# Kernel optimization log

Measured on AMD Instinct MI355X. Metric: run time of the kernel, lower is better.

The kernel has to match this reference:

```python
import jax, jax.numpy as jnp
import numpy as np

N, D, E, TOP_K = 2048, 512, 16, 2
HID = 4 * D
EPS = 1e-10


def setup_inputs() -> dict:
    key = jax.random.key(0)
    ks = jax.random.split(key, 8)
    s = 0.02
    return {
        "x": jax.random.normal(ks[0], (N, D), dtype=jnp.float32),
        "w_norm": jnp.ones((D,), dtype=jnp.float32),
        "Wr": jax.random.normal(ks[1], (D, E), dtype=jnp.float32) * s,
        "br": jnp.zeros((E,), dtype=jnp.float32),
        "W1": jax.random.normal(ks[2], (E, D, HID), dtype=jnp.float32) * s,
        "b1": jnp.zeros((E, HID), dtype=jnp.float32),
        "W2": jax.random.normal(ks[3], (E, HID, D), dtype=jnp.float32) * s,
        "b2": jnp.zeros((E, D), dtype=jnp.float32),
    }


def reference(x, w_norm, Wr, br, W1, b1, W2, b2):
    res = x
    # RMSNorm over feature dim (dim=1 in the torch code for 2D input)
    rms = jnp.sqrt(jnp.mean(x * x, axis=1, keepdims=True) + EPS)
    xn = w_norm * (x / rms)
    # Router: top-k over expert logits, softmax over the k selected logits
    logits = xn @ Wr + br                      # [N, E]
    top_p, top_i = jax.lax.top_k(logits, TOP_K)  # [N, k]
    top_p = jax.nn.softmax(top_p, axis=-1)
    # Dense per-token expert weights [N, E] (top-k indices are distinct)
    weight = jnp.zeros((x.shape[0], E), dtype=x.dtype)
    weight = weight.at[jnp.arange(x.shape[0])[:, None], top_i].add(top_p)
    # All-expert FFN (dense reference for the routed dispatch)
    h = jnp.einsum("nd,edh->enh", xn, W1) + b1[:, None, :]   # [E, N, 4D]
    y = jnp.einsum("enh,ehd->end", jax.nn.silu(h), W2) + b2[:, None, :]  # [E, N, D]
    out = jnp.einsum("end,ne->nd", y, weight)
    return out + res
```

## Files before the change

kernel.cpp:

```cpp
#include <hip/hip_runtime.h>

#define N_TOK 2048
#define DIM   512
#define NEXP  16
#define HID   2048
#define NSLOT (N_TOK*2)

typedef __attribute__((ext_vector_type(8))) short short8;
typedef __attribute__((ext_vector_type(4))) float floatx4;

__device__ __forceinline__ ushort f2bf(float f) {
    union { float f; unsigned u; } c; c.f = f;
    unsigned u = c.u;
    unsigned r = (u + 0x7fffu + ((u >> 16) & 1u)) >> 16;
    return (ushort)r;
}

__device__ __forceinline__ void gl_lds16(const void* g, void* l) {
    __builtin_amdgcn_global_load_lds(
        (const __attribute__((address_space(1))) unsigned int*)g,
        (__attribute__((address_space(3))) unsigned int*)l, 16, 0, 0);
}

__global__ __launch_bounds__(256)
void transpose_convert(const float* __restrict__ src, ushort* __restrict__ dst,
                       int K, int Nn)
{
    const int NT = Nn >> 6, KT = K >> 6;
    int bx = blockIdx.x;
    const int nt = bx % NT; bx /= NT;
    const int kt = bx % KT; bx /= KT;
    const int e  = bx;

    __shared__ float Ls[64 * 65];
    const int t = threadIdx.x;

    const float* sp = src + ((size_t)e * K + kt * 64) * Nn + nt * 64;
#pragma unroll
    for (int i = 0; i < 4; i++) {
        const int k  = (t >> 4) + i * 16;
        const int c4 = (t & 15) * 4;
        const float4 v = *(const float4*)(sp + (size_t)k * Nn + c4);
        Ls[k * 65 + c4 + 0] = v.x;
        Ls[k * 65 + c4 + 1] = v.y;
        Ls[k * 65 + c4 + 2] = v.z;
        Ls[k * 65 + c4 + 3] = v.w;
    }
    __syncthreads();

    ushort* dp = dst + ((size_t)e * Nn + nt * 64) * K + kt * 64;
#pragma unroll
    for (int i = 0; i < 2; i++) {
        const int n = (t >> 3) + i * 32;
        const int c = t & 7;
        unsigned w[4];
#pragma unroll
        for (int q = 0; q < 4; q++) {
            const unsigned lo = f2bf(Ls[(c * 8 + q * 2 + 0) * 65 + n]);
            const unsigned hi = f2bf(Ls[(c * 8 + q * 2 + 1) * 65 + n]);
            w[q] = lo | (hi << 16);
        }
        uint4 o = make_uint4(w[0], w[1], w[2], w[3]);
        *(uint4*)(dp + (size_t)n * K + c * 8) = o;
    }
}

__global__ __launch_bounds__(256)
void router_fused(const float* __restrict__ x, const float* __restrict__ w_norm,
                  const float* __restrict__ Wr, const float* __restrict__ br,
                  ushort* __restrict__ xn, int2* __restrict__ rec_e,
                  float2* __restrict__ rec_w)
{
    __shared__ float xs[16][516];
    __shared__ float wrT[16][516];

    const int tid  = threadIdx.x;
    const int wave = tid >> 6, lane = tid & 63;
    const int tblk = blockIdx.x * 16;

#pragma unroll
    for (int k = 0; k < 32; k++) {
        const int idx = tid + k * 256;
        wrT[idx & 15][idx >> 4] = Wr[idx];
    }

    const float4* wnp = (const float4*)w_norm;
    const float4 wa = wnp[lane], wb = wnp[lane + 64];
#pragma unroll
    for (int i = 0; i < 4; i++) {
        const int tl = wave * 4 + i, t = tblk + tl;
        const float4* xp = (const float4*)(x + (size_t)t * DIM);
        const float4 a = xp[lane], b = xp[lane + 64];
        float ss = a.x*a.x + a.y*a.y + a.z*a.z + a.w*a.w
                 + b.x*b.x + b.y*b.y + b.z*b.z + b.w*b.w;
#pragma unroll
        for (int m = 32; m >= 1; m >>= 1) ss += __shfl_xor(ss, m, 64);
        const float rinv = 1.f / sqrtf(ss * (1.f / (float)DIM) + 1e-10f);
        float4 na, nb;
        na.x = a.x * wa.x * rinv; na.y = a.y * wa.y * rinv;
        na.z = a.z * wa.z * rinv; na.w = a.w * wa.w * rinv;
        nb.x = b.x * wb.x * rinv; nb.y = b.y * wb.y * rinv;
        nb.z = b.z * wb.z * rinv; nb.w = b.w * wb.w * rinv;
        *(float4*)&xs[tl][lane * 4]       = na;
        *(float4*)&xs[tl][256 + lane * 4] = nb;
        ushort4 ua, ub;
        ua.x = f2bf(na.x); ua.y = f2bf(na.y); ua.z = f2bf(na.z); ua.w = f2bf(na.w);
        ub.x = f2bf(nb.x); ub.y = f2bf(nb.y); ub.z = f2bf(nb.z); ub.w = f2bf(nb.w);
        ushort4* xo = (ushort4*)(xn + (size_t)t * DIM);
        xo[lane] = ua; xo[lane + 64] = ub;
    }
    __syncthreads();

    const int tl = tid >> 4, e = tid & 15;
    const int t = tblk + tl;
    float acc = 0.f;
#pragma unroll 4
    for (int d = 0; d < DIM; d += 4) {
        const float4 xv = *(const float4*)&xs[tl][d];
        const float4 wv = *(const float4*)&wrT[e][d];
        acc += xv.x * wv.x + xv.y * wv.y + xv.z * wv.z + xv.w * wv.w;
    }
    const float v = acc + br[e];

    float m0 = v; int i0 = e; float m1 = -1e30f; int i1 = 16;
#pragma unroll
    for (int msk = 1; msk < 16; msk <<= 1) {
        const float om0 = __shfl_xor(m0, msk, 64); const int oi0 = __shfl_xor(i0, msk, 64);
        const float om1 = __shfl_xor(m1, msk, 64); const int oi1 = __shfl_xor(i1, msk, 64);
        const bool bf_ = (om0 > m0) || (om0 == m0 && oi0 < i0);
        const float t0m = bf_ ? om0 : m0; const int t0i = bf_ ? oi0 : i0;
        const float l0m = bf_ ? m0 : om0; const int l0i = bf_ ? i0 : oi0;
        const bool b2_ = (om1 > m1) || (om1 == m1 && oi1 < i1);
        const float t2m = b2_ ? om1 : m1; const int t2i = b2_ ? oi1 : i1;
        const bool lw = (l0m > t2m) || (l0m == t2m && l0i < t2i);
        m0 = t0m; i0 = t0i;
        m1 = lw ? l0m : t2m; i1 = lw ? l0i : t2i;
    }
    if (e == 0) {
        const float ex = expf(m1 - m0);
        const float w0 = 1.f / (1.f + ex);
        rec_e[t] = make_int2(i0, i1);
        rec_w[t] = make_float2(w0, ex * w0);
    }
}

__global__ __launch_bounds__(1024)
void plan_kernel(const int2* __restrict__ rec_e, int* __restrict__ cnt,
                 int* __restrict__ off, int* __restrict__ tok_of_slot,
                 int* __restrict__ rec_slot)
{
    __shared__ int soff[17];
    const int e = threadIdx.x >> 6;
    const int lane = threadIdx.x & 63;

    int total = 0;
    for (int c = 0; c < N_TOK / 64; c++) {
        const int2 er = rec_e[c * 64 + lane];
        const bool hit = (er.x == e) || (er.y == e);
        total += __popcll(__ballot(hit));
    }
    if (lane == 0) soff[e + 1] = total;
    __syncthreads();
    if (threadIdx.x == 0) {
        soff[0] = 0;
        for (int q = 1; q <= 16; q++) soff[q] += soff[q - 1];
    }
    __syncthreads();
    int base = soff[e];
    if (lane == 0) { cnt[e] = soff[e + 1] - base; off[e] = base; }

    for (int c = 0; c < N_TOK / 64; c++) {
        const int t = c * 64 + lane;
        const int2 er = rec_e[t];
        const bool hit = (er.x == e) || (er.y == e);
        const unsigned long long b = __ballot(hit);
        if (hit) {
            const int slot = base + __popcll(b & ((1ull << lane) - 1ull));
            tok_of_slot[slot] = t;
            const int which = (er.y == e) ? 1 : 0;
            rec_slot[t * 2 + which] = slot;
        }
        base += __popcll(b);
    }
}

template<int MODE>
__global__ __launch_bounds__(256)
void gemm_expert(const ushort* __restrict__ A, int a_stride,
                 const ushort* __restrict__ WT, int wt_k,
                 const float* __restrict__ bias,
                 const int* __restrict__ cnt, const int* __restrict__ off,
                 const int* __restrict__ tok_of_slot,
                 ushort* __restrict__ hout, float* __restrict__ yout)
{
    const int flat = blockIdx.x + (blockIdx.y << 5);
    const int x = flat & 7;
    const int g = flat >> 3;
    int e, mt, nb, z;
    if (MODE == 0) {
        e  = x + ((g >> 7) << 3);
        const int r = g & 127;
        nb = r & 31; mt = r >> 5; z = 0;
    } else {
        const int G = ((g >> 5) << 3) + x;
        e = G >> 2; z = G & 3;
        const int idx = g & 31;
        mt = idx >> 3; nb = idx & 7;
    }

    const int count = cnt[e];
    if (mt * 128 >= count) return;
    const int base = off[e];
    const int rows = min(128, count - mt * 128);
    const int n0   = nb * 64;
    const int Nn   = (MODE == 0) ? HID : DIM;
    const int kbeg = (MODE == 0) ? 0 : (z * 512);
    float* yp = (MODE == 0) ? nullptr : (yout + (size_t)z * NSLOT * DIM);

    __shared__ __align__(16) ushort As[2][128 * 64];
    __shared__ __align__(16) ushort Bs[2][64 * 64];
    __shared__ int toks[128];

    const int tid = threadIdx.x;
    if (tid < 128) {
        const int r = tid < rows ? tid : rows - 1;
        const int slot = base + mt * 128 + r;
        toks[tid] = (MODE == 0) ? tok_of_slot[slot] : slot;
    }
    __syncthreads();

    const int lane = tid & 63;
    const int wid  = tid >> 6;
    const int wm = wid >> 1, wn = wid & 1;
    const int fr = lane & 15, fg = lane >> 4;

    const int lrow = lane >> 3;
    const int sch  = (lane & 7) ^ lrow;

    const ushort* aptr[4];
#pragma unroll
    for (int j = 0; j < 4; j++) {
        const int s = wid * 4 + j;
        aptr[j] = A + (size_t)toks[s * 8 + lrow] * a_stride + sch * 8;
    }
    const ushort* wbase = WT + (size_t)e * Nn * wt_k + (size_t)n0 * wt_k;
    const ushort* bptr[2];
#pragma unroll
    for (int j = 0; j < 2; j++) {
        const int s = wid * 2 + j;
        bptr[j] = wbase + (size_t)(s * 8 + lrow) * wt_k + sch * 8;
    }

    floatx4 acc[4][2];
#pragma unroll
    for (int mi = 0; mi < 4; mi++)
#pragma unroll
        for (int ni = 0; ni < 2; ni++)
#pragma unroll
            for (int r = 0; r < 4; r++) acc[mi][ni][r] = 0.f;

#define STAGE(pb, k0)                                                        \
    do {                                                                     \
        _Pragma("unroll")                                                    \
        for (int j = 0; j < 4; j++)                                          \
            gl_lds16(aptr[j] + (k0), (void*)(&As[pb][(wid * 4 + j) * 512])); \
        _Pragma("unroll")                                                    \
        for (int j = 0; j < 2; j++)                                          \
            gl_lds16(bptr[j] + (k0), (void*)(&Bs[pb][(wid * 2 + j) * 512])); \
    } while (0)

    int cur = 0;
    STAGE(0, kbeg);

    for (int kt = 0; kt < 8; kt++) {
        if (kt < 7) {
            STAGE(cur ^ 1, kbeg + (kt + 1) * 64);
            asm volatile("s_waitcnt vmcnt(6)" ::: "memory");
        } else {
            asm volatile("s_waitcnt vmcnt(0)" ::: "memory");
        }
        __builtin_amdgcn_s_barrier();
        __builtin_amdgcn_sched_barrier(0);

#pragma unroll
        for (int kh = 0; kh < 2; kh++) {
            const int co = ((kh * 4 + fg) ^ (fr & 7)) * 8;
            short8 af[4], bfr[2];
#pragma unroll
            for (int mi = 0; mi < 4; mi++)
                af[mi] = *(const short8*)&As[cur][(wm * 64 + mi * 16 + fr) * 64 + co];
#pragma unroll
            for (int ni = 0; ni < 2; ni++)
                bfr[ni] = *(const short8*)&Bs[cur][(wn * 32 + ni * 16 + fr) * 64 + co];
#pragma unroll
            for (int mi = 0; mi < 4; mi++)
#pragma unroll
                for (int ni = 0; ni < 2; ni++)
                    acc[mi][ni] = __builtin_amdgcn_mfma_f32_16x16x32_bf16(af[mi], bfr[ni], acc[mi][ni], 0, 0, 0);
        }

        __builtin_amdgcn_sched_barrier(0);
        __builtin_amdgcn_s_barrier();
        cur ^= 1;
    }
#undef STAGE

#pragma unroll
    for (int ni = 0; ni < 2; ni++) {
        const int gn = n0 + wn * 32 + ni * 16 + fr;
        const float bv = (MODE == 0) ? bias[e * HID + gn] : 0.f;
#pragma unroll
        for (int mi = 0; mi < 4; mi++) {
#pragma unroll
            for (int r = 0; r < 4; r++) {
                const int lm = wm * 64 + mi * 16 + fg * 4 + r;
                if (lm < rows) {
                    const int slot = base + mt * 128 + lm;
                    float v = acc[mi][ni][r];
                    if (MODE == 0) {
                        v += bv;
                        v = v / (1.f + expf(-v));
                        hout[(size_t)slot * HID + gn] = f2bf(v);
                    } else {
                        yp[(size_t)slot * DIM + gn] = v;
                    }
                }
            }
        }
    }
}

__global__ __launch_bounds__(128)
void gather_kernel(const float* __restrict__ x, const float* __restrict__ ypart,
                   const float* __restrict__ b2,
                   const int2* __restrict__ rec_e, const float2* __restrict__ rec_w,
                   const int2* __restrict__ rec_slot, float* __restrict__ out)
{
    const int t = blockIdx.x;
    const int d4 = threadIdx.x * 4;
    const int2 ei = rec_e[t];
    const float2 w = rec_w[t];
    const int2 sl = rec_slot[t];
    const float4 xv  = *(const float4*)(x  + (size_t)t * DIM + d4);
    float4 s0 = make_float4(0.f, 0.f, 0.f, 0.f);
    float4 s1 = make_float4(0.f, 0.f, 0.f, 0.f);
#pragma unroll
    for (int kc = 0; kc < 4; kc++) {
        const float* yp = ypart + (size_t)kc * NSLOT * DIM;
        const float4 a = *(const float4*)(yp + (size_t)sl.x * DIM + d4);
        const float4 b = *(const float4*)(yp + (size_t)sl.y * DIM + d4);
        s0.x += a.x; s0.y += a.y; s0.z += a.z; s0.w += a.w;
        s1.x += b.x; s1.y += b.y; s1.z += b.z; s1.w += b.w;
    }
    const float4 b0  = *(const float4*)(b2 + (size_t)ei.x * DIM + d4);
    const float4 b1v = *(const float4*)(b2 + (size_t)ei.y * DIM + d4);
    float4 o;
    o.x = xv.x + w.x * (s0.x + b0.x) + w.y * (s1.x + b1v.x);
    o.y = xv.y + w.x * (s0.y + b0.y) + w.y * (s1.y + b1v.y);
    o.z = xv.z + w.x * (s0.z + b0.z) + w.y * (s1.z + b1v.z);
    o.w = xv.w + w.x * (s0.w + b0.w) + w.y * (s1.w + b1v.w);
    *(float4*)(out + (size_t)t * DIM + d4) = o;
}

extern "C" void kernel_launch(void* const* d_in, const int* in_sizes, int n_in,
                              void* d_out, int out_size, void* d_ws, size_t ws_size,
                              hipStream_t stream)
{
    const float* x  = (const float*)d_in[0];
    const float* wn = (const float*)d_in[1];
    const float* Wr = (const float*)d_in[2];
    const float* br = (const float*)d_in[3];
    const float* W1 = (const float*)d_in[4];
    const float* b1 = (const float*)d_in[5];
    const float* W2 = (const float*)d_in[6];
    const float* b2 = (const float*)d_in[7];
    float* out = (float*)d_out;

    char* ws = (char*)d_ws;
    ushort* W1T   = (ushort*)(ws);
    ushort* W2T   = (ushort*)(ws + (32u << 20));
    ushort* xn    = (ushort*)(ws + (64u << 20));
    ushort* h_buf = (ushort*)(ws + (66u << 20));
    float*  y_par = (float*) (ws + (82u << 20));
    char* p = ws + (114u << 20);
    int*    cnt         = (int*)p;    p += 256;
    int*    off         = (int*)p;    p += 256;
    int2*   rec_e       = (int2*)p;   p += N_TOK * 8;
    float2* rec_w       = (float2*)p; p += N_TOK * 8;
    int2*   rec_slot    = (int2*)p;   p += N_TOK * 8;
    int*    tok_of_slot = (int*)p;    p += NSLOT * 4;

    router_fused<<<N_TOK / 16, 256, 0, stream>>>(x, wn, Wr, br, xn, rec_e, rec_w);
    plan_kernel<<<1, 1024, 0, stream>>>(rec_e, cnt, off, tok_of_slot, (int*)rec_slot);

    transpose_convert<<<NEXP * 8 * 32, 256, 0, stream>>>(W1, W1T, DIM, HID);
    gemm_expert<0><<<dim3(32, 64), 256, 0, stream>>>(
        xn, DIM, W1T, DIM, b1, cnt, off, tok_of_slot, h_buf, nullptr);

    transpose_convert<<<NEXP * 32 * 8, 256, 0, stream>>>(W2, W2T, HID, DIM);
    gemm_expert<1><<<dim3(32, 64), 256, 0, stream>>>(
        h_buf, HID, W2T, HID, nullptr, cnt, off, nullptr, nullptr, y_par);

    gather_kernel<<<N_TOK, 128, 0, stream>>>(x, y_par, b2, rec_e, rec_w, rec_slot, out);
}
```

Baseline: 119.2 us.

## Halve GEMM K-tile to 32, store split-K partials in bf16, use fast exp

The expert GEMM k-tile drops from 64 to 32, so the loop runs twice as many iterations with half the LDS per stage. The LDS swizzle and the load mapping are reworked to match, and s_setprio is raised around the MFMA block. The split-K partial outputs of the second GEMM are now stored as bf16 instead of fp32, which halves the partial-sum write and read traffic in the gather kernel at some cost in precision. SiLU switches to __expf.

```diff
diff --git a/kernel.cpp b/kernel.cpp
--- a/kernel.cpp
+++ b/kernel.cpp
@@ -14,6 +14,10 @@
     unsigned u = c.u;
     unsigned r = (u + 0x7fffu + ((u >> 16) & 1u)) >> 16;
     return (ushort)r;
+}
+__device__ __forceinline__ float bf2f(ushort u) {
+    union { unsigned u; float f; } c; c.u = ((unsigned)u) << 16;
+    return c.f;
 }
 
 __device__ __forceinline__ void gl_lds16(const void* g, void* l) {
@@ -191,7 +195,7 @@
                  const float* __restrict__ bias,
                  const int* __restrict__ cnt, const int* __restrict__ off,
                  const int* __restrict__ tok_of_slot,
-                 ushort* __restrict__ hout, float* __restrict__ yout)
+                 ushort* __restrict__ hout, ushort* __restrict__ yout)
 {
     const int flat = blockIdx.x + (blockIdx.y << 5);
     const int x = flat & 7;
@@ -215,10 +219,10 @@
     const int n0   = nb * 64;
     const int Nn   = (MODE == 0) ? HID : DIM;
     const int kbeg = (MODE == 0) ? 0 : (z * 512);
-    float* yp = (MODE == 0) ? nullptr : (yout + (size_t)z * NSLOT * DIM);
-
-    __shared__ __align__(16) ushort As[2][128 * 64];
-    __shared__ __align__(16) ushort Bs[2][64 * 64];
+    ushort* yp = (MODE == 0) ? nullptr : (yout + (size_t)z * NSLOT * DIM);
+
+    __shared__ __align__(16) ushort As[2][128 * 32];
+    __shared__ __align__(16) ushort Bs[2][64 * 32];
     __shared__ int toks[128];
 
     const int tid = threadIdx.x;
@@ -234,22 +238,17 @@
     const int wm = wid >> 1, wn = wid & 1;
     const int fr = lane & 15, fg = lane >> 4;
 
-    const int lrow = lane >> 3;
-    const int sch  = (lane & 7) ^ lrow;
-
-    const ushort* aptr[4];
-#pragma unroll
-    for (int j = 0; j < 4; j++) {
-        const int s = wid * 4 + j;
-        aptr[j] = A + (size_t)toks[s * 8 + lrow] * a_stride + sch * 8;
-    }
+    const int rl  = lane >> 2;
+    const int sko = ((lane & 3) ^ ((lane >> 4) & 3)) * 8;
+
+    const ushort* aptr[2];
     const ushort* wbase = WT + (size_t)e * Nn * wt_k + (size_t)n0 * wt_k;
-    const ushort* bptr[2];
 #pragma unroll
     for (int j = 0; j < 2; j++) {
         const int s = wid * 2 + j;
-        bptr[j] = wbase + (size_t)(s * 8 + lrow) * wt_k + sch * 8;
-    }
+        aptr[j] = A + (size_t)toks[s * 16 + rl] * a_stride + sko;
+    }
+    const ushort* bptr = wbase + (size_t)(wid * 16 + rl) * wt_k + sko;
 
     floatx4 acc[4][2];
 #pragma unroll
@@ -262,42 +261,42 @@
 #define STAGE(pb, k0)                                                        \
     do {                                                                     \
         _Pragma("unroll")                                                    \
-        for (int j = 0; j < 4; j++)                                          \
-            gl_lds16(aptr[j] + (k0), (void*)(&As[pb][(wid * 4 + j) * 512])); \
-        _Pragma("unroll")                                                    \
         for (int j = 0; j < 2; j++)                                          \
-            gl_lds16(bptr[j] + (k0), (void*)(&Bs[pb][(wid * 2 + j) * 512])); \
+            gl_lds16(aptr[j] + (k0), (void*)(&As[pb][(wid * 2 + j) * 512])); \
+        gl_lds16(bptr + (k0), (void*)(&Bs[pb][wid * 512]));                  \
     } while (0)
 
     int cur = 0;
     STAGE(0, kbeg);
 
-    for (int kt = 0; kt < 8; kt++) {
-        if (kt < 7) {
-            STAGE(cur ^ 1, kbeg + (kt + 1) * 64);
-            asm volatile("s_waitcnt vmcnt(6)" ::: "memory");
+    const int cxor = (fr >> 2) & 3;
+    for (int kt = 0; kt < 16; kt++) {
+        if (kt < 15) {
+            STAGE(cur ^ 1, kbeg + (kt + 1) * 32);
+            asm volatile("s_waitcnt vmcnt(3)" ::: "memory");
         } else {
             asm volatile("s_waitcnt vmcnt(0)" ::: "memory");
         }
         __builtin_amdgcn_s_barrier();
         __builtin_amdgcn_sched_barrier(0);
 
-#pragma unroll
-        for (int kh = 0; kh < 2; kh++) {
-            const int co = ((kh * 4 + fg) ^ (fr & 7)) * 8;
+        __builtin_amdgcn_s_setprio(1);
+        {
+            const int co = (fg ^ cxor) * 8;
             short8 af[4], bfr[2];
 #pragma unroll
             for (int mi = 0; mi < 4; mi++)
-                af[mi] = *(const short8*)&As[cur][(wm * 64 + mi * 16 + fr) * 64 + co];
+                af[mi] = *(const short8*)&As[cur][(wm * 64 + mi * 16 + fr) * 32 + co];
 #pragma unroll
             for (int ni = 0; ni < 2; ni++)
-                bfr[ni] = *(const short8*)&Bs[cur][(wn * 32 + ni * 16 + fr) * 64 + co];
+                bfr[ni] = *(const short8*)&Bs[cur][(wn * 32 + ni * 16 + fr) * 32 + co];
 #pragma unroll
             for (int mi = 0; mi < 4; mi++)
 #pragma unroll
                 for (int ni = 0; ni < 2; ni++)
                     acc[mi][ni] = __builtin_amdgcn_mfma_f32_16x16x32_bf16(af[mi], bfr[ni], acc[mi][ni], 0, 0, 0);
         }
+        __builtin_amdgcn_s_setprio(0);
 
         __builtin_amdgcn_sched_barrier(0);
         __builtin_amdgcn_s_barrier();
@@ -319,10 +318,10 @@
                     float v = acc[mi][ni][r];
                     if (MODE == 0) {
                         v += bv;
-                        v = v / (1.f + expf(-v));
+                        v = v / (1.f + __expf(-v));
                         hout[(size_t)slot * HID + gn] = f2bf(v);
                     } else {
-                        yp[(size_t)slot * DIM + gn] = v;
+                        yp[(size_t)slot * DIM + gn] = f2bf(v);
                     }
                 }
             }
@@ -331,7 +330,7 @@
 }
 
 __global__ __launch_bounds__(128)
-void gather_kernel(const float* __restrict__ x, const float* __restrict__ ypart,
+void gather_kernel(const float* __restrict__ x, const ushort* __restrict__ ypart,
                    const float* __restrict__ b2,
                    const int2* __restrict__ rec_e, const float2* __restrict__ rec_w,
                    const int2* __restrict__ rec_slot, float* __restrict__ out)
@@ -346,11 +345,11 @@
     float4 s1 = make_float4(0.f, 0.f, 0.f, 0.f);
 #pragma unroll
     for (int kc = 0; kc < 4; kc++) {
-        const float* yp = ypart + (size_t)kc * NSLOT * DIM;
-        const float4 a = *(const float4*)(yp + (size_t)sl.x * DIM + d4);
-        const float4 b = *(const float4*)(yp + (size_t)sl.y * DIM + d4);
-        s0.x += a.x; s0.y += a.y; s0.z += a.z; s0.w += a.w;
-        s1.x += b.x; s1.y += b.y; s1.z += b.z; s1.w += b.w;
+        const ushort* yp = ypart + (size_t)kc * NSLOT * DIM;
+        const ushort4 a = *(const ushort4*)(yp + (size_t)sl.x * DIM + d4);
+        const ushort4 b = *(const ushort4*)(yp + (size_t)sl.y * DIM + d4);
+        s0.x += bf2f(a.x); s0.y += bf2f(a.y); s0.z += bf2f(a.z); s0.w += bf2f(a.w);
+        s1.x += bf2f(b.x); s1.y += bf2f(b.y); s1.z += bf2f(b.z); s1.w += bf2f(b.w);
     }
     const float4 b0  = *(const float4*)(b2 + (size_t)ei.x * DIM + d4);
     const float4 b1v = *(const float4*)(b2 + (size_t)ei.y * DIM + d4);
@@ -381,7 +380,7 @@
     ushort* W2T   = (ushort*)(ws + (32u << 20));
     ushort* xn    = (ushort*)(ws + (64u << 20));
     ushort* h_buf = (ushort*)(ws + (66u << 20));
-    float*  y_par = (float*) (ws + (82u << 20));
+    ushort* y_par = (ushort*)(ws + (82u << 20));
     char* p = ws + (114u << 20);
     int*    cnt         = (int*)p;    p += 256;
     int*    off         = (int*)p;    p += 256;
```

Measured after the change: 117.0 us. Within noise of the previous version (-1.8%).
